# Performance work log

Hardware: AMD Instinct MI355X
Metric: run time of the kernel (lower is better)

## Reference

```python
import jax, jax.numpy as jnp
import numpy as np

NUM_SAMPLES = 2048
MAX_AGENTS = 64
D_MODEL = 128
NUM_HEADS = 8


def setup_inputs() -> dict:
    key = jax.random.key(0)
    # deterministic ragged sizes: 1..64 repeating -> total = 32 * (64*65/2) = 66560
    agents = ((np.arange(NUM_SAMPLES) % MAX_AGENTS) + 1).astype(np.int32)
    total = int(agents.sum())
    k1, k2, k3 = jax.random.split(key, 3)
    s = 1.0 / np.sqrt(D_MODEL)
    return {
        "att_in": jax.random.normal(k1, (total, D_MODEL), jnp.float32),
        "in_proj_w": jax.random.uniform(k2, (3 * D_MODEL, D_MODEL), jnp.float32, -s, s),
        "in_proj_b": jnp.zeros((3 * D_MODEL,), jnp.float32),
        "out_proj_w": jax.random.uniform(k3, (D_MODEL, D_MODEL), jnp.float32, -s, s),
        "out_proj_b": jnp.zeros((D_MODEL,), jnp.float32),
        "agents_per_sample": jnp.asarray(agents),
    }


def reference(att_in, in_proj_w, in_proj_b, out_proj_w, out_proj_b, agents_per_sample):
    # agents_per_sample is static ragged metadata (host ints)
    agents = np.asarray(agents_per_sample)
    B = len(agents)
    A = int(agents.max())
    D = att_in.shape[-1]
    hd = D // NUM_HEADS

    # scatter ragged tokens into zero-padded [B, A, D]
    sample_ids = np.repeat(np.arange(B), agents)
    pos = np.concatenate([np.arange(n) for n in agents])
    padded = jnp.zeros((B, A, D), att_in.dtype).at[sample_ids, pos].set(att_in)
    key_valid = jnp.asarray(np.arange(A)[None, :] < agents[:, None])  # [B, A]

    # torch nn.MultiheadAttention math (eval mode, dropout=0)
    qkv = padded @ in_proj_w.T + in_proj_b  # [B, A, 3D]
    q, k, v = jnp.split(qkv, 3, axis=-1)
    q = q.reshape(B, A, NUM_HEADS, hd)
    k = k.reshape(B, A, NUM_HEADS, hd)
    v = v.reshape(B, A, NUM_HEADS, hd)

    scores = jnp.einsum("bqhd,bkhd->bhqk", q, k) / jnp.sqrt(jnp.asarray(hd, q.dtype))
    scores = jnp.where(key_valid[:, None, None, :], scores, jnp.asarray(-1e30, scores.dtype))
    attn = jax.nn.softmax(scores, axis=-1)

    out = jnp.einsum("bhqk,bkhd->bqhd", attn, v).reshape(B, A, D)
    out = out @ out_proj_w.T + out_proj_b

    # unpad: concatenation of the per-sample ragged outputs
    return out[sample_ids, pos]
```

## Files before the change

kernel.cpp:

```cpp
#include <hip/hip_runtime.h>

#define DM 128
#define NHEADS 8

typedef __attribute__((ext_vector_type(8))) __bf16 bf16x8;
typedef __attribute__((ext_vector_type(8))) unsigned short u16x8;
typedef __attribute__((ext_vector_type(4))) float f32x4;

__device__ inline unsigned short f2bf(float f) {
    unsigned u = __float_as_uint(f);
    u += 0x7FFFu + ((u >> 16) & 1u);
    return (unsigned short)(u >> 16);
}

__global__ void prep(const int* __restrict__ agents, int B,
                     const float* __restrict__ wqkv, const float* __restrict__ wout,
                     int* __restrict__ offs,
                     unsigned short* __restrict__ wqkv_bf,
                     unsigned short* __restrict__ wout_bf) {
    if (blockIdx.x < 64) {
        int idx = (blockIdx.x * 256 + threadIdx.x) * 4;
        if (idx < 49152) {
            float4 v = *(const float4*)(wqkv + idx);
            ushort4 o;
            o.x = f2bf(v.x); o.y = f2bf(v.y); o.z = f2bf(v.z); o.w = f2bf(v.w);
            *(ushort4*)(wqkv_bf + idx) = o;
        } else {
            int j = idx - 49152;
            float4 v = *(const float4*)(wout + j);
            ushort4 o;
            o.x = f2bf(v.x); o.y = f2bf(v.y); o.z = f2bf(v.z); o.w = f2bf(v.w);
            *(ushort4*)(wout_bf + j) = o;
        }
    } else {
        __shared__ int part[256];
        const int tid = threadIdx.x;
        const int per = (B + 255) >> 8;
        const int base = tid * per;
        int s = 0;
        for (int i = 0; i < per; ++i) {
            int idx = base + i;
            if (idx < B) s += agents[idx];
        }
        part[tid] = s;
        __syncthreads();
        for (int off = 1; off < 256; off <<= 1) {
            int v = (tid >= off) ? part[tid - off] : 0;
            __syncthreads();
            part[tid] += v;
            __syncthreads();
        }
        int run = (tid == 0) ? 0 : part[tid - 1];
        for (int i = 0; i < per; ++i) {
            int idx = base + i;
            if (idx < B) { offs[idx] = run; run += agents[idx]; }
        }
    }
}

__launch_bounds__(256, 4)
__global__ void qkv_gemm(const float* __restrict__ x,
                         const unsigned short* __restrict__ wqkvb,
                         const float* __restrict__ bqkv,
                         unsigned short* __restrict__ qws,
                         unsigned short* __restrict__ kv,
                         int M) {
    __shared__ __align__(16) unsigned short Bs[128 * 136];
    __shared__ __align__(16) float biass[128];
    const int bid = blockIdx.x;
    const int seg = bid % 3;
    const int m0 = (bid / 3) * 128;
    const int tid = threadIdx.x;

    for (int f = tid; f < 2048; f += 256) {
        int t = f >> 4, c = f & 15;
        *(uint4*)&Bs[t * 136 + c * 8] =
            *(const uint4*)(wqkvb + (size_t)(seg * 128 + t) * 128 + c * 8);
    }
    if (tid < 32)
        ((float4*)biass)[tid] = ((const float4*)(bqkv + seg * 128))[tid];
    __syncthreads();

    const int wave = tid >> 6, lane = tid & 63, quad = lane >> 4, l16 = lane & 15;
    const int mw = m0 + wave * 32;

    bf16x8 af[2][4];
    #pragma unroll
    for (int mt = 0; mt < 2; ++mt) {
        int row = mw + mt * 16 + l16;
        row = (row < M) ? row : (M - 1);
        const float* xr = x + (size_t)row * DM;
        #pragma unroll
        for (int ks = 0; ks < 4; ++ks) {
            float4 u = *(const float4*)(xr + ks * 32 + quad * 8);
            float4 v = *(const float4*)(xr + ks * 32 + quad * 8 + 4);
            u16x8 t;
            t[0] = f2bf(u.x); t[1] = f2bf(u.y); t[2] = f2bf(u.z); t[3] = f2bf(u.w);
            t[4] = f2bf(v.x); t[5] = f2bf(v.y); t[6] = f2bf(v.z); t[7] = f2bf(v.w);
            af[mt][ks] = __builtin_bit_cast(bf16x8, t);
        }
    }

    unsigned short* obase; int ostride, ocol;
    if (seg == 0) { obase = qws; ostride = 128; ocol = 0; }
    else          { obase = kv;  ostride = 256; ocol = (seg == 2) ? 128 : 0; }

    const int row0 = mw + l16, row1 = row0 + 16;

    for (int ct = 0; ct < 8; ++ct) {
        bf16x8 bc[4];
        #pragma unroll
        for (int ks = 0; ks < 4; ++ks)
            bc[ks] = *(const bf16x8*)&Bs[(ct * 16 + l16) * 136 + ks * 32 + quad * 8];
        f32x4 a0 = {0.f, 0.f, 0.f, 0.f}, a1 = {0.f, 0.f, 0.f, 0.f};
        #pragma unroll
        for (int ks = 0; ks < 4; ++ks) {
            a0 = __builtin_amdgcn_mfma_f32_16x16x32_bf16(bc[ks], af[0][ks], a0, 0, 0, 0);
            a1 = __builtin_amdgcn_mfma_f32_16x16x32_bf16(bc[ks], af[1][ks], a1, 0, 0, 0);
        }
        const int n0 = ct * 16 + quad * 4;
        const float4 b4 = *(const float4*)(biass + n0);
        ushort4 v0, v1;
        v0.x = f2bf(a0[0] + b4.x); v0.y = f2bf(a0[1] + b4.y);
        v0.z = f2bf(a0[2] + b4.z); v0.w = f2bf(a0[3] + b4.w);
        v1.x = f2bf(a1[0] + b4.x); v1.y = f2bf(a1[1] + b4.y);
        v1.z = f2bf(a1[2] + b4.z); v1.w = f2bf(a1[3] + b4.w);
        if (row0 < M) *(ushort4*)(obase + (size_t)row0 * ostride + ocol + n0) = v0;
        if (row1 < M) *(ushort4*)(obase + (size_t)row1 * ostride + ocol + n0) = v1;
    }
}

template<int K4>
__device__ __forceinline__ void attn_body(
    unsigned short* __restrict__ qa,
    const unsigned short* __restrict__ kv,
    int n, int base, int M, int h, int quad, int l16)
{
    bf16x8 kf[K4];
    #pragma unroll
    for (int kt = 0; kt < K4; ++kt) {
        kf[kt] = (bf16x8)(__bf16)0.0f;
        if (quad < 2) {
            int kr = base + kt * 16 + l16;
            kr = kr < M ? kr : M - 1;
            kf[kt] = *(const bf16x8*)(kv + (size_t)kr * 256 + h * 16 + quad * 8);
        }
    }
    bf16x8 vA[K4 / 2];
    #pragma unroll
    for (int g = 0; g < K4 / 2; ++g)
        #pragma unroll
        for (int j = 0; j < 8; ++j) {
            int vr = base + g * 32 + ((j >> 2) * 16) + quad * 4 + (j & 3);
            vr = vr < M ? vr : M - 1;
            vA[g][j] = ((const __bf16*)kv)[(size_t)vr * 256 + 128 + h * 16 + l16];
        }
    int thr[K4];
    #pragma unroll
    for (int kt = 0; kt < K4; ++kt) {
        int t = n - kt * 16 - quad * 4;
        thr[kt] = t < 0 ? 0 : (t > 4 ? 4 : t);
    }
    const float SC2 = 0.25f * 1.44269504088896340736f;
    const int nqt = (n + 15) >> 4;

    int qr0 = base + l16; qr0 = qr0 < M ? qr0 : M - 1;
    bf16x8 qf = (bf16x8)(__bf16)0.0f;
    if (quad < 2) qf = *(const bf16x8*)(qa + (size_t)qr0 * 128 + h * 16 + quad * 8);

    for (int mt = 0; mt < nqt; ++mt) {
        bf16x8 qn = (bf16x8)(__bf16)0.0f;
        if (mt + 1 < nqt && quad < 2) {
            int qr = base + (mt + 1) * 16 + l16;
            qr = qr < M ? qr : M - 1;
            qn = *(const bf16x8*)(qa + (size_t)qr * 128 + h * 16 + quad * 8);
        }
        float pr[K4][4];
        float mm = -3.0e38f;
        #pragma unroll
        for (int kt = 0; kt < K4; ++kt) {
            f32x4 sc = __builtin_amdgcn_mfma_f32_16x16x32_bf16(
                kf[kt], qf, (f32x4){0.f, 0.f, 0.f, 0.f}, 0, 0, 0);
            #pragma unroll
            for (int r = 0; r < 4; ++r) {
                float v = sc[r] * SC2;
                pr[kt][r] = v;
                mm = fmaxf(mm, v);
            }
        }
        mm = fmaxf(mm, __shfl_xor(mm, 16));
        mm = fmaxf(mm, __shfl_xor(mm, 32));
        float ll = 0.f;
        #pragma unroll
        for (int kt = 0; kt < K4; ++kt)
            #pragma unroll
            for (int r = 0; r < 4; ++r) {
                float e = exp2f(pr[kt][r] - mm);
                e = (r < thr[kt]) ? e : 0.f;
                pr[kt][r] = e;
                ll += e;
            }
        ll += __shfl_xor(ll, 16);
        ll += __shfl_xor(ll, 32);
        float inv = __builtin_amdgcn_rcpf(ll);
        bf16x8 pf[K4 / 2];
        #pragma unroll
        for (int g = 0; g < K4 / 2; ++g)
            #pragma unroll
            for (int j = 0; j < 8; ++j)
                pf[g][j] = (__bf16)(pr[2 * g + (j >> 2)][j & 3] * inv);
        f32x4 o = __builtin_amdgcn_mfma_f32_16x16x32_bf16(
            vA[0], pf[0], (f32x4){0.f, 0.f, 0.f, 0.f}, 0, 0, 0);
        if (K4 == 4)
            o = __builtin_amdgcn_mfma_f32_16x16x32_bf16(vA[1], pf[1], o, 0, 0, 0);
        const int row = mt * 16 + l16;
        if (row < n) {
            ushort4 w;
            w.x = f2bf(o[0]); w.y = f2bf(o[1]); w.z = f2bf(o[2]); w.w = f2bf(o[3]);
            *(ushort4*)(qa + (size_t)(base + row) * 128 + h * 16 + quad * 4) = w;
        }
        qf = qn;
    }
}

__launch_bounds__(512, 6)
__global__ void attn(unsigned short* __restrict__ qa,
                     const unsigned short* __restrict__ kv,
                     const int* __restrict__ agents,
                     const int* __restrict__ offs,
                     int M) {
    const int s = blockIdx.x;
    const int n = agents[s];
    const int base = offs[s];
    const int tid = threadIdx.x;
    const int h = tid >> 6, lane = tid & 63, quad = (lane >> 4), l16 = lane & 15;
    (void)lane;
    if (n > 32) attn_body<4>(qa, kv, n, base, M, h, quad, l16);
    else        attn_body<2>(qa, kv, n, base, M, h, quad, l16);
}

__launch_bounds__(256, 4)
__global__ void oproj(const unsigned short* __restrict__ attn_b,
                      const unsigned short* __restrict__ woutb,
                      const float* __restrict__ bout,
                      float* __restrict__ out, int M) {
    __shared__ __align__(16) unsigned short Ws[128 * 136];
    __shared__ __align__(16) float biass[128];
    const int m0 = blockIdx.x * 64;
    const int tid = threadIdx.x;

    for (int f = tid; f < 2048; f += 256) {
        int t = f >> 4, c = f & 15;
        *(uint4*)&Ws[t * 136 + c * 8] = *(const uint4*)(woutb + (size_t)t * 128 + c * 8);
    }
    if (tid < 32)
        ((float4*)biass)[tid] = ((const float4*)bout)[tid];
    __syncthreads();

    const int wave = tid >> 6, lane = tid & 63, quad = lane >> 4, l16 = lane & 15;
    const int mw = m0 + wave * 16;

    bf16x8 af[4];
    {
        int row = mw + l16;
        row = (row < M) ? row : (M - 1);
        #pragma unroll
        for (int ks = 0; ks < 4; ++ks)
            af[ks] = *(const bf16x8*)(attn_b + (size_t)row * DM + ks * 32 + quad * 8);
    }

    const int row0 = mw + l16;

    for (int ct = 0; ct < 8; ++ct) {
        bf16x8 bc[4];
        #pragma unroll
        for (int ks = 0; ks < 4; ++ks)
            bc[ks] = *(const bf16x8*)&Ws[(ct * 16 + l16) * 136 + ks * 32 + quad * 8];
        f32x4 a0 = {0.f, 0.f, 0.f, 0.f};
        #pragma unroll
        for (int ks = 0; ks < 4; ++ks)
            a0 = __builtin_amdgcn_mfma_f32_16x16x32_bf16(bc[ks], af[ks], a0, 0, 0, 0);
        const int n0 = ct * 16 + quad * 4;
        const float4 b4 = *(const float4*)(biass + n0);
        float4 o0;
        o0.x = a0[0] + b4.x; o0.y = a0[1] + b4.y; o0.z = a0[2] + b4.z; o0.w = a0[3] + b4.w;
        if (row0 < M) *(float4*)(out + (size_t)row0 * DM + n0) = o0;
    }
}

extern "C" void kernel_launch(void* const* d_in, const int* in_sizes, int n_in,
                              void* d_out, int out_size, void* d_ws, size_t ws_size,
                              hipStream_t stream) {
    const float* att_in     = (const float*)d_in[0];
    const float* in_proj_w  = (const float*)d_in[1];
    const float* in_proj_b  = (const float*)d_in[2];
    const float* out_proj_w = (const float*)d_in[3];
    const float* out_proj_b = (const float*)d_in[4];
    const int*   agents     = (const int*)d_in[5];
    const int B = in_sizes[5];
    const int M = out_size / DM;

    int* offs = (int*)d_ws;
    unsigned short* wqkv_bf = (unsigned short*)((char*)d_ws + 8192);
    unsigned short* wout_bf = (unsigned short*)((char*)d_ws + 106496);
    unsigned short* qbuf    = (unsigned short*)((char*)d_ws + 139264);
    unsigned short* kvbuf   = (unsigned short*)d_out;

    const int strips = (M + 127) / 128;

    hipLaunchKernelGGL(prep, dim3(65), dim3(256), 0, stream,
                       agents, B, in_proj_w, out_proj_w, offs, wqkv_bf, wout_bf);
    hipLaunchKernelGGL(qkv_gemm, dim3(strips * 3), dim3(256), 0, stream,
                       att_in, wqkv_bf, in_proj_b, qbuf, kvbuf, M);
    hipLaunchKernelGGL(attn, dim3(B), dim3(512), 0, stream,
                       qbuf, kvbuf, agents, offs, M);
    hipLaunchKernelGGL(oproj, dim3((M + 63) / 64), dim3(256), 0, stream,
                       qbuf, wout_bf, out_proj_b, (float*)d_out, M);
}
```

Before: 159.0 us.

## Fuse QKV projection, attention and output projection into one per-sample kernel

Replaces the three kernels (QKV GEMM, per-sample attention, output projection) with one kernel per sample. It stages that sample's input rows in LDS as bf16, and each wave computes its head's Q/K/V using weights read from global memory, with Q/K passed through lane shuffles and V kept in LDS. Attention output goes to LDS, and the output projection is applied before writing float results. This removes the global round trips for the Q/K/V and attention intermediates and two launches. In exchange it reloads the weight slices per sample block, adds per-sample template dispatch on tile count, and does padded GEMM work on tiles for small samples.

```diff
diff --git a/kernel.cpp b/kernel.cpp
--- a/kernel.cpp
+++ b/kernel.cpp
@@ -58,141 +58,99 @@
     }
 }
 
-__launch_bounds__(256, 4)
-__global__ void qkv_gemm(const float* __restrict__ x,
-                         const unsigned short* __restrict__ wqkvb,
-                         const float* __restrict__ bqkv,
-                         unsigned short* __restrict__ qws,
-                         unsigned short* __restrict__ kv,
-                         int M) {
-    __shared__ __align__(16) unsigned short Bs[128 * 136];
-    __shared__ __align__(16) float biass[128];
-    const int bid = blockIdx.x;
-    const int seg = bid % 3;
-    const int m0 = (bid / 3) * 128;
-    const int tid = threadIdx.x;
-
-    for (int f = tid; f < 2048; f += 256) {
-        int t = f >> 4, c = f & 15;
-        *(uint4*)&Bs[t * 136 + c * 8] =
-            *(const uint4*)(wqkvb + (size_t)(seg * 128 + t) * 128 + c * 8);
-    }
-    if (tid < 32)
-        ((float4*)biass)[tid] = ((const float4*)(bqkv + seg * 128))[tid];
+template<int NT>
+__device__ __forceinline__ void fused_body(
+    const unsigned short* __restrict__ wqkvb, const float* __restrict__ bqkv,
+    const unsigned short* __restrict__ woutb, const float* __restrict__ bout,
+    float* __restrict__ out,
+    unsigned short* __restrict__ Xs, unsigned short* __restrict__ Vs,
+    int n, int base, int h, int quad, int l16)
+{
+    constexpr int G   = (NT + 1) / 2;
+    constexpr int KT2 = 2 * G;
+    bf16x8 qf[NT], kf[NT];
+    const int shA = (quad & 1) * 32 + l16;
+    const int shB = shA + 16;
+
+    #pragma unroll
+    for (int seg = 0; seg < 3; ++seg) {
+        bf16x8 wf[4];
+        #pragma unroll
+        for (int ks = 0; ks < 4; ++ks)
+            wf[ks] = *(const bf16x8*)(wqkvb +
+                     (size_t)(seg * 128 + h * 16 + l16) * 128 + ks * 32 + quad * 8);
+        const float4 bs = *(const float4*)(bqkv + seg * 128 + h * 16 + quad * 4);
+        #pragma unroll
+        for (int mt = 0; mt < NT; ++mt) {
+            f32x4 acc = {0.f, 0.f, 0.f, 0.f};
+            #pragma unroll
+            for (int ks = 0; ks < 4; ++ks) {
+                bf16x8 xf = *(const bf16x8*)&Xs[(mt * 16 + l16) * 136 + ks * 32 + quad * 8];
+                acc = __builtin_amdgcn_mfma_f32_16x16x32_bf16(wf[ks], xf, acc, 0, 0, 0);
+            }
+            ushort4 w;
+            w.x = f2bf(acc[0] + bs.x); w.y = f2bf(acc[1] + bs.y);
+            w.z = f2bf(acc[2] + bs.z); w.w = f2bf(acc[3] + bs.w);
+            if (seg == 2) {
+                *(ushort4*)&Vs[(mt * 16 + l16) * 136 + h * 16 + quad * 4] = w;
+            } else {
+                unsigned u0 = (unsigned)w.x | ((unsigned)w.y << 16);
+                unsigned u1 = (unsigned)w.z | ((unsigned)w.w << 16);
+                uint4 q;
+                q.x = __shfl(u0, shA); q.y = __shfl(u1, shA);
+                q.z = __shfl(u0, shB); q.w = __shfl(u1, shB);
+                bf16x8 fr = (quad < 2) ? __builtin_bit_cast(bf16x8, q)
+                                       : (bf16x8)(__bf16)0.0f;
+                if (seg == 0) qf[mt] = fr; else kf[mt] = fr;
+            }
+        }
+    }
+
+    bf16x8 vA[G];
+    const __bf16* Vsb = (const __bf16*)Vs;
+    #pragma unroll
+    for (int g = 0; g < G; ++g)
+        #pragma unroll
+        for (int j = 0; j < 8; ++j)
+            vA[g][j] = Vsb[(size_t)(g * 32 + ((j >> 2) * 16) + quad * 4 + (j & 3)) * 136
+                           + h * 16 + l16];
+
     __syncthreads();
 
-    const int wave = tid >> 6, lane = tid & 63, quad = lane >> 4, l16 = lane & 15;
-    const int mw = m0 + wave * 32;
-
-    bf16x8 af[2][4];
-    #pragma unroll
-    for (int mt = 0; mt < 2; ++mt) {
-        int row = mw + mt * 16 + l16;
-        row = (row < M) ? row : (M - 1);
-        const float* xr = x + (size_t)row * DM;
-        #pragma unroll
-        for (int ks = 0; ks < 4; ++ks) {
-            float4 u = *(const float4*)(xr + ks * 32 + quad * 8);
-            float4 v = *(const float4*)(xr + ks * 32 + quad * 8 + 4);
-            u16x8 t;
-            t[0] = f2bf(u.x); t[1] = f2bf(u.y); t[2] = f2bf(u.z); t[3] = f2bf(u.w);
-            t[4] = f2bf(v.x); t[5] = f2bf(v.y); t[6] = f2bf(v.z); t[7] = f2bf(v.w);
-            af[mt][ks] = __builtin_bit_cast(bf16x8, t);
-        }
-    }
-
-    unsigned short* obase; int ostride, ocol;
-    if (seg == 0) { obase = qws; ostride = 128; ocol = 0; }
-    else          { obase = kv;  ostride = 256; ocol = (seg == 2) ? 128 : 0; }
-
-    const int row0 = mw + l16, row1 = row0 + 16;
-
-    for (int ct = 0; ct < 8; ++ct) {
-        bf16x8 bc[4];
-        #pragma unroll
-        for (int ks = 0; ks < 4; ++ks)
-            bc[ks] = *(const bf16x8*)&Bs[(ct * 16 + l16) * 136 + ks * 32 + quad * 8];
-        f32x4 a0 = {0.f, 0.f, 0.f, 0.f}, a1 = {0.f, 0.f, 0.f, 0.f};
-        #pragma unroll
-        for (int ks = 0; ks < 4; ++ks) {
-            a0 = __builtin_amdgcn_mfma_f32_16x16x32_bf16(bc[ks], af[0][ks], a0, 0, 0, 0);
-            a1 = __builtin_amdgcn_mfma_f32_16x16x32_bf16(bc[ks], af[1][ks], a1, 0, 0, 0);
-        }
-        const int n0 = ct * 16 + quad * 4;
-        const float4 b4 = *(const float4*)(biass + n0);
-        ushort4 v0, v1;
-        v0.x = f2bf(a0[0] + b4.x); v0.y = f2bf(a0[1] + b4.y);
-        v0.z = f2bf(a0[2] + b4.z); v0.w = f2bf(a0[3] + b4.w);
-        v1.x = f2bf(a1[0] + b4.x); v1.y = f2bf(a1[1] + b4.y);
-        v1.z = f2bf(a1[2] + b4.z); v1.w = f2bf(a1[3] + b4.w);
-        if (row0 < M) *(ushort4*)(obase + (size_t)row0 * ostride + ocol + n0) = v0;
-        if (row1 < M) *(ushort4*)(obase + (size_t)row1 * ostride + ocol + n0) = v1;
-    }
-}
-
-template<int K4>
-__device__ __forceinline__ void attn_body(
-    unsigned short* __restrict__ qa,
-    const unsigned short* __restrict__ kv,
-    int n, int base, int M, int h, int quad, int l16)
-{
-    bf16x8 kf[K4];
-    #pragma unroll
-    for (int kt = 0; kt < K4; ++kt) {
-        kf[kt] = (bf16x8)(__bf16)0.0f;
-        if (quad < 2) {
-            int kr = base + kt * 16 + l16;
-            kr = kr < M ? kr : M - 1;
-            kf[kt] = *(const bf16x8*)(kv + (size_t)kr * 256 + h * 16 + quad * 8);
-        }
-    }
-    bf16x8 vA[K4 / 2];
-    #pragma unroll
-    for (int g = 0; g < K4 / 2; ++g)
-        #pragma unroll
-        for (int j = 0; j < 8; ++j) {
-            int vr = base + g * 32 + ((j >> 2) * 16) + quad * 4 + (j & 3);
-            vr = vr < M ? vr : M - 1;
-            vA[g][j] = ((const __bf16*)kv)[(size_t)vr * 256 + 128 + h * 16 + l16];
-        }
-    int thr[K4];
-    #pragma unroll
-    for (int kt = 0; kt < K4; ++kt) {
+    int thr[KT2];
+    #pragma unroll
+    for (int kt = 0; kt < KT2; ++kt) {
         int t = n - kt * 16 - quad * 4;
         thr[kt] = t < 0 ? 0 : (t > 4 ? 4 : t);
     }
     const float SC2 = 0.25f * 1.44269504088896340736f;
-    const int nqt = (n + 15) >> 4;
-
-    int qr0 = base + l16; qr0 = qr0 < M ? qr0 : M - 1;
-    bf16x8 qf = (bf16x8)(__bf16)0.0f;
-    if (quad < 2) qf = *(const bf16x8*)(qa + (size_t)qr0 * 128 + h * 16 + quad * 8);
-
-    for (int mt = 0; mt < nqt; ++mt) {
-        bf16x8 qn = (bf16x8)(__bf16)0.0f;
-        if (mt + 1 < nqt && quad < 2) {
-            int qr = base + (mt + 1) * 16 + l16;
-            qr = qr < M ? qr : M - 1;
-            qn = *(const bf16x8*)(qa + (size_t)qr * 128 + h * 16 + quad * 8);
-        }
-        float pr[K4][4];
+    unsigned short* Os = Xs;
+
+    #pragma unroll
+    for (int mt = 0; mt < NT; ++mt) {
+        float pr[KT2][4];
         float mm = -3.0e38f;
         #pragma unroll
-        for (int kt = 0; kt < K4; ++kt) {
-            f32x4 sc = __builtin_amdgcn_mfma_f32_16x16x32_bf16(
-                kf[kt], qf, (f32x4){0.f, 0.f, 0.f, 0.f}, 0, 0, 0);
-            #pragma unroll
-            for (int r = 0; r < 4; ++r) {
-                float v = sc[r] * SC2;
-                pr[kt][r] = v;
-                mm = fmaxf(mm, v);
+        for (int kt = 0; kt < KT2; ++kt) {
+            if (kt < NT) {
+                f32x4 sc = __builtin_amdgcn_mfma_f32_16x16x32_bf16(
+                    kf[kt], qf[mt], (f32x4){0.f, 0.f, 0.f, 0.f}, 0, 0, 0);
+                #pragma unroll
+                for (int r = 0; r < 4; ++r) {
+                    float v = sc[r] * SC2;
+                    pr[kt][r] = v;
+                    mm = fmaxf(mm, v);
+                }
+            } else {
+                #pragma unroll
+                for (int r = 0; r < 4; ++r) pr[kt][r] = -3.0e38f;
             }
         }
         mm = fmaxf(mm, __shfl_xor(mm, 16));
         mm = fmaxf(mm, __shfl_xor(mm, 32));
         float ll = 0.f;
         #pragma unroll
-        for (int kt = 0; kt < K4; ++kt)
+        for (int kt = 0; kt < KT2; ++kt)
             #pragma unroll
             for (int r = 0; r < 4; ++r) {
                 float e = exp2f(pr[kt][r] - mm);
@@ -203,89 +161,90 @@
         ll += __shfl_xor(ll, 16);
         ll += __shfl_xor(ll, 32);
         float inv = __builtin_amdgcn_rcpf(ll);
-        bf16x8 pf[K4 / 2];
-        #pragma unroll
-        for (int g = 0; g < K4 / 2; ++g)
+        bf16x8 pf[G];
+        #pragma unroll
+        for (int g = 0; g < G; ++g)
             #pragma unroll
             for (int j = 0; j < 8; ++j)
                 pf[g][j] = (__bf16)(pr[2 * g + (j >> 2)][j & 3] * inv);
         f32x4 o = __builtin_amdgcn_mfma_f32_16x16x32_bf16(
             vA[0], pf[0], (f32x4){0.f, 0.f, 0.f, 0.f}, 0, 0, 0);
-        if (K4 == 4)
+        if constexpr (G == 2)
             o = __builtin_amdgcn_mfma_f32_16x16x32_bf16(vA[1], pf[1], o, 0, 0, 0);
         const int row = mt * 16 + l16;
         if (row < n) {
             ushort4 w;
             w.x = f2bf(o[0]); w.y = f2bf(o[1]); w.z = f2bf(o[2]); w.w = f2bf(o[3]);
-            *(ushort4*)(qa + (size_t)(base + row) * 128 + h * 16 + quad * 4) = w;
-        }
-        qf = qn;
-    }
-}
-
-__launch_bounds__(512, 6)
-__global__ void attn(unsigned short* __restrict__ qa,
-                     const unsigned short* __restrict__ kv,
-                     const int* __restrict__ agents,
-                     const int* __restrict__ offs,
-                     int M) {
+            *(ushort4*)&Os[row * 136 + h * 16 + quad * 4] = w;
+        }
+    }
+    __syncthreads();
+
+    bf16x8 wf2[4];
+    #pragma unroll
+    for (int ks = 0; ks < 4; ++ks)
+        wf2[ks] = *(const bf16x8*)(woutb +
+                  (size_t)(h * 16 + l16) * 128 + ks * 32 + quad * 8);
+    const float4 bo = *(const float4*)(bout + h * 16 + quad * 4);
+    #pragma unroll
+    for (int mt = 0; mt < NT; ++mt) {
+        const int row = mt * 16 + l16;
+        f32x4 acc = {0.f, 0.f, 0.f, 0.f};
+        #pragma unroll
+        for (int ks = 0; ks < 4; ++ks) {
+            bf16x8 af = *(const bf16x8*)&Os[row * 136 + ks * 32 + quad * 8];
+            acc = __builtin_amdgcn_mfma_f32_16x16x32_bf16(wf2[ks], af, acc, 0, 0, 0);
+        }
+        if (row < n) {
+            float4 o;
+            o.x = acc[0] + bo.x; o.y = acc[1] + bo.y;
+            o.z = acc[2] + bo.z; o.w = acc[3] + bo.w;
+            *(float4*)(out + (size_t)(base + row) * DM + h * 16 + quad * 4) = o;
+        }
+    }
+}
+
+#define XS_OFF 0
+#define VS_OFF 17408
+#define SMEMF  34816
+
+__launch_bounds__(512, 4)
+__global__ void fused(const float* __restrict__ x,
+                      const unsigned short* __restrict__ wqkvb,
+                      const float* __restrict__ bqkv,
+                      const unsigned short* __restrict__ woutb,
+                      const float* __restrict__ bout,
+                      float* __restrict__ out,
+                      const int* __restrict__ agents,
+                      const int* __restrict__ offs) {
+    __shared__ __align__(16) char smem[SMEMF];
+    unsigned short* Xs = (unsigned short*)(smem + XS_OFF);
+    unsigned short* Vs = (unsigned short*)(smem + VS_OFF);
+
     const int s = blockIdx.x;
     const int n = agents[s];
     const int base = offs[s];
     const int tid = threadIdx.x;
-    const int h = tid >> 6, lane = tid & 63, quad = (lane >> 4), l16 = lane & 15;
-    (void)lane;
-    if (n > 32) attn_body<4>(qa, kv, n, base, M, h, quad, l16);
-    else        attn_body<2>(qa, kv, n, base, M, h, quad, l16);
-}
-
-__launch_bounds__(256, 4)
-__global__ void oproj(const unsigned short* __restrict__ attn_b,
-                      const unsigned short* __restrict__ woutb,
-                      const float* __restrict__ bout,
-                      float* __restrict__ out, int M) {
-    __shared__ __align__(16) unsigned short Ws[128 * 136];
-    __shared__ __align__(16) float biass[128];
-    const int m0 = blockIdx.x * 64;
-    const int tid = threadIdx.x;
-
-    for (int f = tid; f < 2048; f += 256) {
-        int t = f >> 4, c = f & 15;
-        *(uint4*)&Ws[t * 136 + c * 8] = *(const uint4*)(woutb + (size_t)t * 128 + c * 8);
-    }
-    if (tid < 32)
-        ((float4*)biass)[tid] = ((const float4*)bout)[tid];
+    const int h = tid >> 6, lane = tid & 63, quad = lane >> 4, l16 = lane & 15;
+
+    for (int f = tid; f < 1088; f += 512)
+        ((uint4*)(smem + VS_OFF))[f] = make_uint4(0u, 0u, 0u, 0u);
+    for (int f = tid; f < 2048; f += 512) {
+        int t = f >> 5, c = f & 31;
+        ushort4 o = make_ushort4(0, 0, 0, 0);
+        if (t < n) {
+            float4 v = *(const float4*)(x + (size_t)(base + t) * DM + c * 4);
+            o.x = f2bf(v.x); o.y = f2bf(v.y); o.z = f2bf(v.z); o.w = f2bf(v.w);
+        }
+        *(ushort4*)&Xs[t * 136 + c * 4] = o;
+    }
     __syncthreads();
 
-    const int wave = tid >> 6, lane = tid & 63, quad = lane >> 4, l16 = lane & 15;
-    const int mw = m0 + wave * 16;
-
-    bf16x8 af[4];
-    {
-        int row = mw + l16;
-        row = (row < M) ? row : (M - 1);
-        #pragma unroll
-        for (int ks = 0; ks < 4; ++ks)
-            af[ks] = *(const bf16x8*)(attn_b + (size_t)row * DM + ks * 32 + quad * 8);
-    }
-
-    const int row0 = mw + l16;
-
-    for (int ct = 0; ct < 8; ++ct) {
-        bf16x8 bc[4];
-        #pragma unroll
-        for (int ks = 0; ks < 4; ++ks)
-            bc[ks] = *(const bf16x8*)&Ws[(ct * 16 + l16) * 136 + ks * 32 + quad * 8];
-        f32x4 a0 = {0.f, 0.f, 0.f, 0.f};
-        #pragma unroll
-        for (int ks = 0; ks < 4; ++ks)
-            a0 = __builtin_amdgcn_mfma_f32_16x16x32_bf16(bc[ks], af[ks], a0, 0, 0, 0);
-        const int n0 = ct * 16 + quad * 4;
-        const float4 b4 = *(const float4*)(biass + n0);
-        float4 o0;
-        o0.x = a0[0] + b4.x; o0.y = a0[1] + b4.y; o0.z = a0[2] + b4.z; o0.w = a0[3] + b4.w;
-        if (row0 < M) *(float4*)(out + (size_t)row0 * DM + n0) = o0;
-    }
+    const int nkt = (n + 15) >> 4;
+    if      (nkt == 1) fused_body<1>(wqkvb, bqkv, woutb, bout, out, Xs, Vs, n, base, h, quad, l16);
+    else if (nkt == 2) fused_body<2>(wqkvb, bqkv, woutb, bout, out, Xs, Vs, n, base, h, quad, l16);
+    else if (nkt == 3) fused_body<3>(wqkvb, bqkv, woutb, bout, out, Xs, Vs, n, base, h, quad, l16);
+    else               fused_body<4>(wqkvb, bqkv, woutb, bout, out, Xs, Vs, n, base, h, quad, l16);
 }
 
 extern "C" void kernel_launch(void* const* d_in, const int* in_sizes, int n_in,
@@ -298,22 +257,14 @@
     const float* out_proj_b = (const float*)d_in[4];
     const int*   agents     = (const int*)d_in[5];
     const int B = in_sizes[5];
-    const int M = out_size / DM;
 
     int* offs = (int*)d_ws;
     unsigned short* wqkv_bf = (unsigned short*)((char*)d_ws + 8192);
     unsigned short* wout_bf = (unsigned short*)((char*)d_ws + 106496);
-    unsigned short* qbuf    = (unsigned short*)((char*)d_ws + 139264);
-    unsigned short* kvbuf   = (unsigned short*)d_out;
-
-    const int strips = (M + 127) / 128;
 
     hipLaunchKernelGGL(prep, dim3(65), dim3(256), 0, stream,
                        agents, B, in_proj_w, out_proj_w, offs, wqkv_bf, wout_bf);
-    hipLaunchKernelGGL(qkv_gemm, dim3(strips * 3), dim3(256), 0, stream,
-                       att_in, wqkv_bf, in_proj_b, qbuf, kvbuf, M);
-    hipLaunchKernelGGL(attn, dim3(B), dim3(512), 0, stream,
-                       qbuf, kvbuf, agents, offs, M);
-    hipLaunchKernelGGL(oproj, dim3((M + 63) / 64), dim3(256), 0, stream,
-                       qbuf, wout_bf, out_proj_b, (float*)d_out, M);
-}
+    hipLaunchKernelGGL(fused, dim3(B), dim3(512), 0, stream,
+                       att_in, wqkv_bf, in_proj_b, wout_bf, out_proj_b,
+                       (float*)d_out, agents, offs);
+}
```

After: 149.0 us. 1.07x faster.
